# Kernel optimization log

Measured on AMD Instinct MI355X. Metric: run time of the kernel, lower is better.

## Reference

```python
import jax, jax.numpy as jnp
import numpy as np

N, E, D_IN, D_HID, D_OUT = 100000, 1600000, 128, 128, 40

def _sage_pool(x, src, dst, Wp, bp, Ws, Wn, b, n_nodes):
    # DGL SAGEConv 'pool': h_pool = relu(fc_pool(x)); h_neigh = max over in-neighbors;
    # out = fc_self(x) + fc_neigh(h_neigh) + bias
    hp = jax.nn.relu(x @ Wp + bp)                       # [N, d]
    msg = hp[src]                                        # [E, d] gather
    agg = jax.ops.segment_max(msg, dst, num_segments=n_nodes)  # [N, d] scatter-max
    agg = jnp.where(jnp.isfinite(agg), agg, 0.0)         # zero-in-degree nodes -> 0
    return x @ Ws + agg @ Wn + b

def setup_inputs() -> dict:
    key = jax.random.key(0)
    ks = jax.random.split(key, 14)
    def lin(k, i, o):
        return jax.random.normal(k, (i, o), dtype=jnp.float32) / np.sqrt(i)
    return {
        "in_feat": jax.random.normal(ks[0], (N, D_IN), dtype=jnp.float32),
        "src": jax.random.randint(ks[1], (E,), 0, N),
        "dst": jax.random.randint(ks[2], (E,), 0, N),
        "Wp1": lin(ks[3], D_IN, D_IN), "bp1": jnp.zeros((D_IN,), jnp.float32),
        "Ws1": lin(ks[4], D_IN, D_HID), "Wn1": lin(ks[5], D_IN, D_HID),
        "b1": jnp.zeros((D_HID,), jnp.float32),
        "Wp2": lin(ks[6], D_HID, D_HID), "bp2": jnp.zeros((D_HID,), jnp.float32),
        "Ws2": lin(ks[7], D_HID, D_OUT), "Wn2": lin(ks[8], D_HID, D_OUT),
        "b2": jnp.zeros((D_OUT,), jnp.float32),
    }

def reference(in_feat, src, dst, Wp1, bp1, Ws1, Wn1, b1, Wp2, bp2, Ws2, Wn2, b2):
    h = _sage_pool(in_feat, src, dst, Wp1, bp1, Ws1, Wn1, b1, N)
    h = jax.nn.relu(h)
    # dropout is identity at inference (eval mode)
    return _sage_pool(h, src, dst, Wp2, bp2, Ws2, Wn2, b2, N)
```

## Files before the change

kernel.cpp:

```cpp
#include <hip/hip_runtime.h>
#include <stdint.h>

#define NN 100000
#define NE 1600000
#define NB 391

using u16 = unsigned short;
using u32 = unsigned int;

typedef __attribute__((ext_vector_type(8))) short bf16x8;
typedef __attribute__((ext_vector_type(4))) float f32x4;

__device__ inline u16 f2b(float f){
  u32 u = __float_as_uint(f);
  u32 r = (u + 0x7fffu + ((u >> 16) & 1u)) >> 16;
  return (u16)r;
}

__global__ void k_prep(const float* __restrict__ Wp1, const float* __restrict__ Ws1,
                       const float* __restrict__ Wn1, const float* __restrict__ Wp2,
                       const float* __restrict__ Ws2, const float* __restrict__ Wn2,
                       u16* __restrict__ wpT1, u16* __restrict__ wc1T,
                       u16* __restrict__ wpT2, u16* __restrict__ wc2T){
  int i = blockIdx.x * 256 + threadIdx.x;
  if (i < 16384){ int n = i >> 7, k = i & 127;
    wpT1[n*128 + k] = f2b(Wp1[k*128 + n]);
    wpT2[n*128 + k] = f2b(Wp2[k*128 + n]);
  }
  if (i < 32768){ int n = i >> 8, k = i & 255;
    float v = (k < 128) ? Ws1[k*128 + n] : Wn1[(k-128)*128 + n];
    wc1T[n*256 + k] = f2b(v);
  }
  if (i < 12288){ int n = i >> 8, k = i & 255;
    float v = 0.f;
    if (n < 40) v = (k < 128) ? Ws2[k*40 + n] : Wn2[(k-128)*40 + n];
    wc2T[n*256 + k] = f2b(v);
  }
}

__global__ __launch_bounds__(256) void k_cb_hist(const int* __restrict__ dst,
                                                 int* __restrict__ cb){
  __shared__ int h[NB];
  for (int i = threadIdx.x; i < NB; i += 256) h[i] = 0;
  __syncthreads();
  int e0 = blockIdx.x * 8192;
  #pragma unroll 4
  for (int j = 0; j < 32; j++){
    int e = e0 + j * 256 + threadIdx.x;
    if (e < NE) atomicAdd(&h[dst[e] >> 8], 1);
  }
  __syncthreads();
  for (int i = threadIdx.x; i < NB; i += 256)
    if (h[i]) atomicAdd(&cb[i], h[i]);
}

__global__ void k_cb_scan(const int* __restrict__ cb, int* __restrict__ cbo,
                          int* __restrict__ curB){
  if (threadIdx.x == 0 && blockIdx.x == 0){
    int a = 0;
    for (int i = 0; i < NB; i++){ cbo[i] = a; curB[i] = a; a += cb[i]; }
    cbo[NB] = a;
  }
}

__global__ __launch_bounds__(256) void k_part(const int* __restrict__ src,
                                              const int* __restrict__ dst,
                                              int* __restrict__ curB,
                                              int2* __restrict__ part){
  __shared__ int hist[NB], scn[NB], cur[NB], base[NB];
  __shared__ int2 stage[4096];
  const int tid = threadIdx.x;
  const int e0 = blockIdx.x * 4096;
  const int cnt = min(4096, NE - e0);
  for (int i = tid; i < NB; i += 256) hist[i] = 0;
  __syncthreads();
  int2 ed[16];
  #pragma unroll
  for (int j = 0; j < 16; j++){
    int e = e0 + j * 256 + tid;
    if (e < NE){
      ed[j].x = src[e]; ed[j].y = dst[e];
      atomicAdd(&hist[ed[j].y >> 8], 1);
    }
  }
  __syncthreads();
  for (int i = tid; i < NB; i += 256)
    base[i] = hist[i] ? atomicAdd(&curB[i], hist[i]) : 0;
  if (tid == 0){
    int a = 0;
    for (int i = 0; i < NB; i++){ scn[i] = a; cur[i] = a; a += hist[i]; }
  }
  __syncthreads();
  #pragma unroll
  for (int j = 0; j < 16; j++){
    int e = e0 + j * 256 + tid;
    if (e < NE){
      int slot = atomicAdd(&cur[ed[j].y >> 8], 1);
      stage[slot] = ed[j];
    }
  }
  __syncthreads();
  for (int i = tid; i < cnt; i += 256){
    int2 p = stage[i];
    int b = p.y >> 8;
    part[base[b] + (i - scn[b])] = p;
  }
}

__global__ __launch_bounds__(256) void k_bsort(const int2* __restrict__ part,
                                               const int* __restrict__ cbo,
                                               int* __restrict__ rp,
                                               int* __restrict__ esrc){
  __shared__ int cnt[256], sc[256], cur[256];
  const int tid = threadIdx.x;
  const int b = blockIdx.x;
  const int lo = cbo[b], hi = cbo[b + 1];
  cnt[tid] = 0;
  __syncthreads();
  for (int i = lo + tid; i < hi; i += 256)
    atomicAdd(&cnt[part[i].y & 255], 1);
  __syncthreads();
  sc[tid] = cnt[tid];
  __syncthreads();
  #pragma unroll
  for (int off = 1; off < 256; off <<= 1){
    int t = (tid >= off) ? sc[tid - off] : 0;
    __syncthreads();
    sc[tid] += t;
    __syncthreads();
  }
  int ex = sc[tid] - cnt[tid];
  int n = (b << 8) + tid;
  if (n < NN) rp[n] = lo + ex;
  if (b == NB - 1 && tid == 0) rp[NN] = hi;
  cur[tid] = lo + ex;
  __syncthreads();
  for (int i = lo + tid; i < hi; i += 256){
    int2 p = part[i];
    int pos = atomicAdd(&cur[p.y & 255], 1);
    esrc[pos] = p.x;
  }
}

__global__ void k_agg(const u16* __restrict__ hp, const int* __restrict__ rp,
                      const int* __restrict__ esrc, u16* __restrict__ agg){
  int node = blockIdx.x * 4 + (threadIdx.x >> 6);
  if (node >= NN) return;
  const int lane = threadIdx.x & 63;
  const int half = lane >> 5;
  const int l32  = lane & 31;
  const int lo = rp[node], hi = rp[node + 1];
  u32 m0 = 0, m1 = 0;
  for (int i = lo; i < hi; i += 16){
    int s[8];
    #pragma unroll
    for (int j = 0; j < 8; j++){
      int ii = i + 2 * j + half; if (ii >= hi) ii = hi - 1;
      s[j] = esrc[ii];
    }
    uint2 v[8];
    #pragma unroll
    for (int j = 0; j < 8; j++)
      v[j] = *(const uint2*)&hp[(size_t)s[j] * 128 + l32 * 4];
    #pragma unroll
    for (int j = 0; j < 8; j++){
      asm("v_pk_max_u16 %0, %0, %1" : "+v"(m0) : "v"(v[j].x));
      asm("v_pk_max_u16 %0, %0, %1" : "+v"(m1) : "v"(v[j].y));
    }
  }
  u32 t0 = (u32)__shfl_xor((int)m0, 32);
  u32 t1 = (u32)__shfl_xor((int)m1, 32);
  asm("v_pk_max_u16 %0, %0, %1" : "+v"(m0) : "v"(t0));
  asm("v_pk_max_u16 %0, %0, %1" : "+v"(m1) : "v"(t1));
  if (half == 0)
    *(uint2*)&agg[(size_t)node * 128 + l32 * 4] = make_uint2(m0, m1);
}

template<int K, int NOUT, int NOUTR, int BM, int NT,
         bool A1F32, bool HASA2, bool RELU, bool OUTF32>
__global__ __launch_bounds__(NT)
void k_gemm(const void* __restrict__ A1p, const u16* __restrict__ A2,
            const u16* __restrict__ Wt, const float* __restrict__ bias,
            void* __restrict__ outp)
{
  constexpr int KSTEP = 64;
  constexpr int KP = KSTEP + 8;
  constexpr int NTI = NOUT / 16;
  __shared__ u16 A_lds[BM * KP];
  __shared__ u16 W_lds[NOUT * KP];
  const int tid  = threadIdx.x;
  const int row0 = blockIdx.x * BM;
  const int wave = tid >> 6, lane = tid & 63;
  const int koff = (lane >> 4) * 8;
  const u16* Ar = &A_lds[(wave * 16 + (lane & 15)) * KP];

  f32x4 acc[NTI] = {};

  #pragma unroll
  for (int k0 = 0; k0 < K; k0 += KSTEP){
    if (k0) __syncthreads();
    for (int c = tid; c < NOUT * 8; c += NT){
      int n = c >> 3, kc = c & 7;
      *(uint4*)&W_lds[n * KP + kc * 8] = *(const uint4*)&Wt[n * K + k0 + kc * 8];
    }
    if (A1F32 && k0 < 128){
      const float* A = (const float*)A1p;
      for (int c = tid; c < BM * 16; c += NT){
        int rl = c >> 4, kc = c & 15;
        int gr = row0 + rl;
        float4 v = make_float4(0.f, 0.f, 0.f, 0.f);
        if (gr < NN) v = *(const float4*)&A[(size_t)gr * 128 + k0 + kc * 4];
        ushort4 o; o.x = f2b(v.x); o.y = f2b(v.y); o.z = f2b(v.z); o.w = f2b(v.w);
        *(ushort4*)&A_lds[rl * KP + kc * 4] = o;
      }
    } else {
      const u16* A = (HASA2 && k0 >= 128) ? A2 : (const u16*)A1p;
      int cb = (HASA2 && k0 >= 128) ? (k0 - 128) : k0;
      for (int c = tid; c < BM * 8; c += NT){
        int rl = c >> 3, kc = c & 7;
        int gr = row0 + rl;
        uint4 v = make_uint4(0, 0, 0, 0);
        if (gr < NN) v = *(const uint4*)&A[(size_t)gr * 128 + cb + kc * 8];
        *(uint4*)&A_lds[rl * KP + kc * 8] = v;
      }
    }
    __syncthreads();

    bf16x8 af0 = *(const bf16x8*)&Ar[koff];
    bf16x8 af1 = *(const bf16x8*)&Ar[32 + koff];
    #pragma unroll
    for (int nt = 0; nt < NTI; nt++){
      const u16* Wr = &W_lds[(nt * 16 + (lane & 15)) * KP];
      bf16x8 b0 = *(const bf16x8*)&Wr[koff];
      bf16x8 b1 = *(const bf16x8*)&Wr[32 + koff];
      acc[nt] = __builtin_amdgcn_mfma_f32_16x16x32_bf16(af0, b0, acc[nt], 0, 0, 0);
      acc[nt] = __builtin_amdgcn_mfma_f32_16x16x32_bf16(af1, b1, acc[nt], 0, 0, 0);
    }
  }

  const int colb = lane & 15;
  const int rowl = wave * 16 + ((lane >> 4) << 2);
  #pragma unroll
  for (int nt = 0; nt < NTI; nt++){
    int col = nt * 16 + colb;
    if (col >= NOUTR) continue;
    float bv = bias[col];
    #pragma unroll
    for (int r = 0; r < 4; r++){
      int gr = row0 + rowl + r;
      if (gr >= NN) continue;
      float v = acc[nt][r] + bv;
      if (RELU) v = fmaxf(v, 0.f);
      if (OUTF32) ((float*)outp)[(size_t)gr * NOUTR + col] = v;
      else        ((u16*)outp)[(size_t)gr * NOUTR + col] = f2b(v);
    }
  }
}

extern "C" void kernel_launch(void* const* d_in, const int* in_sizes, int n_in,
                              void* d_out, int out_size, void* d_ws, size_t ws_size,
                              hipStream_t stream){
  const float* x   = (const float*)d_in[0];
  const int*   src = (const int*)d_in[1];
  const int*   dst = (const int*)d_in[2];
  const float* Wp1 = (const float*)d_in[3];
  const float* bp1 = (const float*)d_in[4];
  const float* Ws1 = (const float*)d_in[5];
  const float* Wn1 = (const float*)d_in[6];
  const float* b1  = (const float*)d_in[7];
  const float* Wp2 = (const float*)d_in[8];
  const float* bp2 = (const float*)d_in[9];
  const float* Ws2 = (const float*)d_in[10];
  const float* Wn2 = (const float*)d_in[11];
  const float* b2  = (const float*)d_in[12];

  char* ws = (char*)d_ws;
  u16* wpT1 = (u16*)(ws + 0);
  u16* wc1T = (u16*)(ws + 32768);
  u16* wpT2 = (u16*)(ws + 98304);
  u16* wc2T = (u16*)(ws + 131072);
  int* cb   = (int*)(ws + 155648);
  int* cbo  = (int*)(ws + 157696);
  int* curB = (int*)(ws + 159744);
  int* rp   = (int*)(ws + 161792);
  int2* part= (int2*)(ws + 561920);
  u16* h    = (u16*)(ws + 561920);
  int* esrc = (int*)(ws + 26161920);
  u16* hp   = (u16*)(ws + 32561920);
  u16* agg  = (u16*)(ws + 58161920);

  hipMemsetAsync(cb, 0, NB * sizeof(int), stream);
  k_prep<<<128, 256, 0, stream>>>(Wp1, Ws1, Wn1, Wp2, Ws2, Wn2, wpT1, wc1T, wpT2, wc2T);
  k_cb_hist<<<(NE + 8191) / 8192, 256, 0, stream>>>(dst, cb);
  k_cb_scan<<<1, 64, 0, stream>>>(cb, cbo, curB);
  k_part<<<(NE + 4095) / 4096, 256, 0, stream>>>(src, dst, curB, part);
  k_bsort<<<NB, 256, 0, stream>>>(part, cbo, rp, esrc);

  k_gemm<128,128,128, 64,256, true ,false,true ,false>
      <<<(NN + 63) / 64, 256, 0, stream>>>(x, nullptr, wpT1, bp1, hp);
  k_agg<<<(NN + 3) / 4, 256, 0, stream>>>(hp, rp, esrc, agg);
  k_gemm<256,128,128,128,512, true ,true ,true ,false>
      <<<(NN + 127) / 128, 512, 0, stream>>>(x, agg, wc1T, b1, h);
  k_gemm<128,128,128, 64,256, false,false,true ,false>
      <<<(NN + 63) / 64, 256, 0, stream>>>(h, nullptr, wpT2, bp2, hp);
  k_agg<<<(NN + 3) / 4, 256, 0, stream>>>(hp, rp, esrc, agg);
  k_gemm<256, 48, 40,128,512, false,true ,false,true >
      <<<(NN + 127) / 128, 512, 0, stream>>>(h, agg, wc2T, b2, d_out);
}
```

Baseline: 284.1 us.

## Fuse neighbor max-aggregation into the combine GEMM through LDS

The separate gather/segment-max kernel is removed. Each combine-GEMM block now computes the max-aggregated neighbor features for its 128 rows straight into shared memory, then consumes them as the second half of K. This removes the agg buffer's global write and re-read and one launch per layer. In exchange the block carries more LDS (an extra 128x136 tile), and the irregular gather latency now runs inside the GEMM block, with each wave looping serially over its 16 nodes, which may lower occupancy and latency hiding.

```diff
diff --git a/kernel.cpp b/kernel.cpp
--- a/kernel.cpp
+++ b/kernel.cpp
@@ -142,46 +142,11 @@
   }
 }
 
-__global__ void k_agg(const u16* __restrict__ hp, const int* __restrict__ rp,
-                      const int* __restrict__ esrc, u16* __restrict__ agg){
-  int node = blockIdx.x * 4 + (threadIdx.x >> 6);
-  if (node >= NN) return;
-  const int lane = threadIdx.x & 63;
-  const int half = lane >> 5;
-  const int l32  = lane & 31;
-  const int lo = rp[node], hi = rp[node + 1];
-  u32 m0 = 0, m1 = 0;
-  for (int i = lo; i < hi; i += 16){
-    int s[8];
-    #pragma unroll
-    for (int j = 0; j < 8; j++){
-      int ii = i + 2 * j + half; if (ii >= hi) ii = hi - 1;
-      s[j] = esrc[ii];
-    }
-    uint2 v[8];
-    #pragma unroll
-    for (int j = 0; j < 8; j++)
-      v[j] = *(const uint2*)&hp[(size_t)s[j] * 128 + l32 * 4];
-    #pragma unroll
-    for (int j = 0; j < 8; j++){
-      asm("v_pk_max_u16 %0, %0, %1" : "+v"(m0) : "v"(v[j].x));
-      asm("v_pk_max_u16 %0, %0, %1" : "+v"(m1) : "v"(v[j].y));
-    }
-  }
-  u32 t0 = (u32)__shfl_xor((int)m0, 32);
-  u32 t1 = (u32)__shfl_xor((int)m1, 32);
-  asm("v_pk_max_u16 %0, %0, %1" : "+v"(m0) : "v"(t0));
-  asm("v_pk_max_u16 %0, %0, %1" : "+v"(m1) : "v"(t1));
-  if (half == 0)
-    *(uint2*)&agg[(size_t)node * 128 + l32 * 4] = make_uint2(m0, m1);
-}
-
 template<int K, int NOUT, int NOUTR, int BM, int NT,
-         bool A1F32, bool HASA2, bool RELU, bool OUTF32>
+         bool A1F32, bool RELU, bool OUTF32>
 __global__ __launch_bounds__(NT)
-void k_gemm(const void* __restrict__ A1p, const u16* __restrict__ A2,
-            const u16* __restrict__ Wt, const float* __restrict__ bias,
-            void* __restrict__ outp)
+void k_gemm(const void* __restrict__ A1p, const u16* __restrict__ Wt,
+            const float* __restrict__ bias, void* __restrict__ outp)
 {
   constexpr int KSTEP = 64;
   constexpr int KP = KSTEP + 8;
@@ -203,7 +168,7 @@
       int n = c >> 3, kc = c & 7;
       *(uint4*)&W_lds[n * KP + kc * 8] = *(const uint4*)&Wt[n * K + k0 + kc * 8];
     }
-    if (A1F32 && k0 < 128){
+    if (A1F32){
       const float* A = (const float*)A1p;
       for (int c = tid; c < BM * 16; c += NT){
         int rl = c >> 4, kc = c & 15;
@@ -214,13 +179,12 @@
         *(ushort4*)&A_lds[rl * KP + kc * 4] = o;
       }
     } else {
-      const u16* A = (HASA2 && k0 >= 128) ? A2 : (const u16*)A1p;
-      int cb = (HASA2 && k0 >= 128) ? (k0 - 128) : k0;
+      const u16* A = (const u16*)A1p;
       for (int c = tid; c < BM * 8; c += NT){
         int rl = c >> 3, kc = c & 7;
         int gr = row0 + rl;
         uint4 v = make_uint4(0, 0, 0, 0);
-        if (gr < NN) v = *(const uint4*)&A[(size_t)gr * 128 + cb + kc * 8];
+        if (gr < NN) v = *(const uint4*)&A[(size_t)gr * 128 + k0 + kc * 8];
         *(uint4*)&A_lds[rl * KP + kc * 8] = v;
       }
     }
@@ -228,6 +192,130 @@
 
     bf16x8 af0 = *(const bf16x8*)&Ar[koff];
     bf16x8 af1 = *(const bf16x8*)&Ar[32 + koff];
+    #pragma unroll
+    for (int nt = 0; nt < NTI; nt++){
+      const u16* Wr = &W_lds[(nt * 16 + (lane & 15)) * KP];
+      bf16x8 b0 = *(const bf16x8*)&Wr[koff];
+      bf16x8 b1 = *(const bf16x8*)&Wr[32 + koff];
+      acc[nt] = __builtin_amdgcn_mfma_f32_16x16x32_bf16(af0, b0, acc[nt], 0, 0, 0);
+      acc[nt] = __builtin_amdgcn_mfma_f32_16x16x32_bf16(af1, b1, acc[nt], 0, 0, 0);
+    }
+  }
+
+  const int colb = lane & 15;
+  const int rowl = wave * 16 + ((lane >> 4) << 2);
+  #pragma unroll
+  for (int nt = 0; nt < NTI; nt++){
+    int col = nt * 16 + colb;
+    if (col >= NOUTR) continue;
+    float bv = bias[col];
+    #pragma unroll
+    for (int r = 0; r < 4; r++){
+      int gr = row0 + rowl + r;
+      if (gr >= NN) continue;
+      float v = acc[nt][r] + bv;
+      if (RELU) v = fmaxf(v, 0.f);
+      if (OUTF32) ((float*)outp)[(size_t)gr * NOUTR + col] = v;
+      else        ((u16*)outp)[(size_t)gr * NOUTR + col] = f2b(v);
+    }
+  }
+}
+
+template<int NOUT, int NOUTR, bool A1F32, bool RELU, bool OUTF32>
+__global__ __launch_bounds__(512)
+void k_fgemm(const void* __restrict__ A1p, const u16* __restrict__ hp,
+             const int* __restrict__ rp, const int* __restrict__ esrc,
+             const u16* __restrict__ Wt, const float* __restrict__ bias,
+             void* __restrict__ outp)
+{
+  constexpr int BM = 128, NT = 512, KSTEP = 64;
+  constexpr int KP  = KSTEP + 8;
+  constexpr int KP2 = 136;
+  constexpr int NTI = NOUT / 16;
+  __shared__ u16 A_lds[BM * KP];
+  __shared__ u16 W_lds[NOUT * KP];
+  __shared__ u16 G_lds[BM * KP2];
+  const int tid  = threadIdx.x;
+  const int row0 = blockIdx.x * BM;
+  const int wave = tid >> 6, lane = tid & 63;
+  const int half = lane >> 5, l32 = lane & 31;
+  const int koff = (lane >> 4) * 8;
+
+  for (int j = 0; j < 16; j++){
+    int node = row0 + wave * 16 + j;
+    u32 m0 = 0, m1 = 0;
+    if (node < NN){
+      int lo = rp[node], hi = rp[node + 1];
+      for (int i = lo; i < hi; i += 16){
+        int s[8];
+        #pragma unroll
+        for (int t = 0; t < 8; t++){
+          int ii = i + 2 * t + half; if (ii >= hi) ii = hi - 1;
+          s[t] = esrc[ii];
+        }
+        uint2 v[8];
+        #pragma unroll
+        for (int t = 0; t < 8; t++)
+          v[t] = *(const uint2*)&hp[(size_t)s[t] * 128 + l32 * 4];
+        #pragma unroll
+        for (int t = 0; t < 8; t++){
+          asm("v_pk_max_u16 %0, %0, %1" : "+v"(m0) : "v"(v[t].x));
+          asm("v_pk_max_u16 %0, %0, %1" : "+v"(m1) : "v"(v[t].y));
+        }
+      }
+    }
+    u32 t0 = (u32)__shfl_xor((int)m0, 32);
+    u32 t1 = (u32)__shfl_xor((int)m1, 32);
+    asm("v_pk_max_u16 %0, %0, %1" : "+v"(m0) : "v"(t0));
+    asm("v_pk_max_u16 %0, %0, %1" : "+v"(m1) : "v"(t1));
+    if (half == 0)
+      *(uint2*)&G_lds[(wave * 16 + j) * KP2 + l32 * 4] = make_uint2(m0, m1);
+  }
+
+  const u16* Ar = &A_lds[(wave * 16 + (lane & 15)) * KP];
+  const u16* Gr = &G_lds[(wave * 16 + (lane & 15)) * KP2];
+
+  f32x4 acc[NTI] = {};
+
+  #pragma unroll
+  for (int k0 = 0; k0 < 256; k0 += KSTEP){
+    if (k0) __syncthreads();
+    for (int c = tid; c < NOUT * 8; c += NT){
+      int n = c >> 3, kc = c & 7;
+      *(uint4*)&W_lds[n * KP + kc * 8] = *(const uint4*)&Wt[n * 256 + k0 + kc * 8];
+    }
+    if (k0 < 128){
+      if (A1F32){
+        const float* A = (const float*)A1p;
+        for (int c = tid; c < BM * 16; c += NT){
+          int rl = c >> 4, kc = c & 15;
+          int gr = row0 + rl;
+          float4 v = make_float4(0.f, 0.f, 0.f, 0.f);
+          if (gr < NN) v = *(const float4*)&A[(size_t)gr * 128 + k0 + kc * 4];
+          ushort4 o; o.x = f2b(v.x); o.y = f2b(v.y); o.z = f2b(v.z); o.w = f2b(v.w);
+          *(ushort4*)&A_lds[rl * KP + kc * 4] = o;
+        }
+      } else {
+        const u16* A = (const u16*)A1p;
+        for (int c = tid; c < BM * 8; c += NT){
+          int rl = c >> 3, kc = c & 7;
+          int gr = row0 + rl;
+          uint4 v = make_uint4(0, 0, 0, 0);
+          if (gr < NN) v = *(const uint4*)&A[(size_t)gr * 128 + k0 + kc * 8];
+          *(uint4*)&A_lds[rl * KP + kc * 8] = v;
+        }
+      }
+    }
+    __syncthreads();
+
+    bf16x8 af0, af1;
+    if (k0 < 128){
+      af0 = *(const bf16x8*)&Ar[koff];
+      af1 = *(const bf16x8*)&Ar[32 + koff];
+    } else {
+      af0 = *(const bf16x8*)&Gr[(k0 - 128) + koff];
+      af1 = *(const bf16x8*)&Gr[(k0 - 128) + 32 + koff];
+    }
     #pragma unroll
     for (int nt = 0; nt < NTI; nt++){
       const u16* Wr = &W_lds[(nt * 16 + (lane & 15)) * KP];
@@ -287,7 +375,6 @@
   u16* h    = (u16*)(ws + 561920);
   int* esrc = (int*)(ws + 26161920);
   u16* hp   = (u16*)(ws + 32561920);
-  u16* agg  = (u16*)(ws + 58161920);
 
   hipMemsetAsync(cb, 0, NB * sizeof(int), stream);
   k_prep<<<128, 256, 0, stream>>>(Wp1, Ws1, Wn1, Wp2, Ws2, Wn2, wpT1, wc1T, wpT2, wc2T);
@@ -296,14 +383,12 @@
   k_part<<<(NE + 4095) / 4096, 256, 0, stream>>>(src, dst, curB, part);
   k_bsort<<<NB, 256, 0, stream>>>(part, cbo, rp, esrc);
 
-  k_gemm<128,128,128, 64,256, true ,false,true ,false>
-      <<<(NN + 63) / 64, 256, 0, stream>>>(x, nullptr, wpT1, bp1, hp);
-  k_agg<<<(NN + 3) / 4, 256, 0, stream>>>(hp, rp, esrc, agg);
-  k_gemm<256,128,128,128,512, true ,true ,true ,false>
-      <<<(NN + 127) / 128, 512, 0, stream>>>(x, agg, wc1T, b1, h);
-  k_gemm<128,128,128, 64,256, false,false,true ,false>
-      <<<(NN + 63) / 64, 256, 0, stream>>>(h, nullptr, wpT2, bp2, hp);
-  k_agg<<<(NN + 3) / 4, 256, 0, stream>>>(hp, rp, esrc, agg);
-  k_gemm<256, 48, 40,128,512, false,true ,false,true >
-      <<<(NN + 127) / 128, 512, 0, stream>>>(h, agg, wc2T, b2, d_out);
-}
+  k_gemm<128,128,128, 64,256, true ,true ,false>
+      <<<(NN + 63) / 64, 256, 0, stream>>>(x, wpT1, bp1, hp);
+  k_fgemm<128,128, true ,true ,false>
+      <<<(NN + 127) / 128, 512, 0, stream>>>(x, hp, rp, esrc, wc1T, b1, h);
+  k_gemm<128,128,128, 64,256, false,true ,false>
+      <<<(NN + 63) / 64, 256, 0, stream>>>(h, wpT2, bp2, hp);
+  k_fgemm< 48, 40, false,false,true >
+      <<<(NN + 127) / 128, 512, 0, stream>>>(h, hp, rp, esrc, wc2T, b2, d_out);
+}
```

Result: slower. 302.8 us (+6.6%).

## Fuse layer-1 combine GEMM with layer-2 pool GEMM and coarsen CSR buckets

Applied to the files above, without the earlier changes.

Adds a fused kernel that computes h = relu(x@Ws1 + agg@Wn1 + b1), keeps the tile in LDS, and immediately applies the layer-2 pool projection to write hp. This removes one GEMM launch and the re-read of h from global memory. The CSR build also moves to 512-node buckets with parallel LDS scans in place of serial single-thread scans, and the memset is folded into the prep kernel. The first pool GEMM now uses 128-row tiles. The risk is higher register pressure in the fused kernel, and its second-GEMM weight fragments are read directly from global memory.

```diff
diff --git a/kernel.cpp b/kernel.cpp
--- a/kernel.cpp
+++ b/kernel.cpp
@@ -3,7 +3,7 @@
 
 #define NN 100000
 #define NE 1600000
-#define NB 391
+#define NB 196
 
 using u16 = unsigned short;
 using u32 = unsigned int;
@@ -21,8 +21,10 @@
                        const float* __restrict__ Wn1, const float* __restrict__ Wp2,
                        const float* __restrict__ Ws2, const float* __restrict__ Wn2,
                        u16* __restrict__ wpT1, u16* __restrict__ wc1T,
-                       u16* __restrict__ wpT2, u16* __restrict__ wc2T){
+                       u16* __restrict__ wpT2, u16* __restrict__ wc2T,
+                       int* __restrict__ cb){
   int i = blockIdx.x * 256 + threadIdx.x;
+  if (i < NB) cb[i] = 0;
   if (i < 16384){ int n = i >> 7, k = i & 127;
     wpT1[n*128 + k] = f2b(Wp1[k*128 + n]);
     wpT2[n*128 + k] = f2b(Wp2[k*128 + n]);
@@ -47,32 +49,43 @@
   #pragma unroll 4
   for (int j = 0; j < 32; j++){
     int e = e0 + j * 256 + threadIdx.x;
-    if (e < NE) atomicAdd(&h[dst[e] >> 8], 1);
+    if (e < NE) atomicAdd(&h[dst[e] >> 9], 1);
   }
   __syncthreads();
   for (int i = threadIdx.x; i < NB; i += 256)
     if (h[i]) atomicAdd(&cb[i], h[i]);
 }
 
-__global__ void k_cb_scan(const int* __restrict__ cb, int* __restrict__ cbo,
-                          int* __restrict__ curB){
-  if (threadIdx.x == 0 && blockIdx.x == 0){
-    int a = 0;
-    for (int i = 0; i < NB; i++){ cbo[i] = a; curB[i] = a; a += cb[i]; }
-    cbo[NB] = a;
-  }
+__global__ __launch_bounds__(256) void k_cb_scan(const int* __restrict__ cb,
+                                                 int* __restrict__ cbo,
+                                                 int* __restrict__ curB){
+  __shared__ int s[256];
+  int tid = threadIdx.x;
+  int v = (tid < NB) ? cb[tid] : 0;
+  s[tid] = v;
+  __syncthreads();
+  #pragma unroll
+  for (int off = 1; off < 256; off <<= 1){
+    int t = (tid >= off) ? s[tid - off] : 0;
+    __syncthreads();
+    s[tid] += t;
+    __syncthreads();
+  }
+  int ex = s[tid] - v;
+  if (tid < NB){ cbo[tid] = ex; curB[tid] = ex; }
+  if (tid == 255) cbo[NB] = s[255];
 }
 
 __global__ __launch_bounds__(256) void k_part(const int* __restrict__ src,
                                               const int* __restrict__ dst,
                                               int* __restrict__ curB,
                                               int2* __restrict__ part){
-  __shared__ int hist[NB], scn[NB], cur[NB], base[NB];
+  __shared__ int hist[256], scn[256], cur[256], base[256];
   __shared__ int2 stage[4096];
   const int tid = threadIdx.x;
   const int e0 = blockIdx.x * 4096;
   const int cnt = min(4096, NE - e0);
-  for (int i = tid; i < NB; i += 256) hist[i] = 0;
+  hist[tid] = 0;
   __syncthreads();
   int2 ed[16];
   #pragma unroll
@@ -80,64 +93,72 @@
     int e = e0 + j * 256 + tid;
     if (e < NE){
       ed[j].x = src[e]; ed[j].y = dst[e];
-      atomicAdd(&hist[ed[j].y >> 8], 1);
-    }
-  }
-  __syncthreads();
-  for (int i = tid; i < NB; i += 256)
-    base[i] = hist[i] ? atomicAdd(&curB[i], hist[i]) : 0;
-  if (tid == 0){
-    int a = 0;
-    for (int i = 0; i < NB; i++){ scn[i] = a; cur[i] = a; a += hist[i]; }
-  }
+      atomicAdd(&hist[ed[j].y >> 9], 1);
+    }
+  }
+  __syncthreads();
+  int hv = hist[tid];
+  base[tid] = (tid < NB && hv) ? atomicAdd(&curB[tid], hv) : 0;
+  scn[tid] = hv;
+  __syncthreads();
+  #pragma unroll
+  for (int off = 1; off < 256; off <<= 1){
+    int t = (tid >= off) ? scn[tid - off] : 0;
+    __syncthreads();
+    scn[tid] += t;
+    __syncthreads();
+  }
+  int ex = scn[tid] - hv;
+  scn[tid] = ex;
+  cur[tid] = ex;
   __syncthreads();
   #pragma unroll
   for (int j = 0; j < 16; j++){
     int e = e0 + j * 256 + tid;
     if (e < NE){
-      int slot = atomicAdd(&cur[ed[j].y >> 8], 1);
+      int slot = atomicAdd(&cur[ed[j].y >> 9], 1);
       stage[slot] = ed[j];
     }
   }
   __syncthreads();
   for (int i = tid; i < cnt; i += 256){
     int2 p = stage[i];
-    int b = p.y >> 8;
+    int b = p.y >> 9;
     part[base[b] + (i - scn[b])] = p;
   }
 }
 
-__global__ __launch_bounds__(256) void k_bsort(const int2* __restrict__ part,
+__global__ __launch_bounds__(512) void k_bsort(const int2* __restrict__ part,
                                                const int* __restrict__ cbo,
                                                int* __restrict__ rp,
                                                int* __restrict__ esrc){
-  __shared__ int cnt[256], sc[256], cur[256];
+  __shared__ int cnt[512], sc[512], cur[512];
   const int tid = threadIdx.x;
   const int b = blockIdx.x;
   const int lo = cbo[b], hi = cbo[b + 1];
   cnt[tid] = 0;
   __syncthreads();
-  for (int i = lo + tid; i < hi; i += 256)
-    atomicAdd(&cnt[part[i].y & 255], 1);
+  for (int i = lo + tid; i < hi; i += 512)
+    atomicAdd(&cnt[part[i].y & 511], 1);
   __syncthreads();
   sc[tid] = cnt[tid];
   __syncthreads();
   #pragma unroll
-  for (int off = 1; off < 256; off <<= 1){
+  for (int off = 1; off < 512; off <<= 1){
     int t = (tid >= off) ? sc[tid - off] : 0;
     __syncthreads();
     sc[tid] += t;
     __syncthreads();
   }
   int ex = sc[tid] - cnt[tid];
-  int n = (b << 8) + tid;
+  int n = (b << 9) + tid;
   if (n < NN) rp[n] = lo + ex;
   if (b == NB - 1 && tid == 0) rp[NN] = hi;
   cur[tid] = lo + ex;
   __syncthreads();
-  for (int i = lo + tid; i < hi; i += 256){
+  for (int i = lo + tid; i < hi; i += 512){
     int2 p = part[i];
-    int pos = atomicAdd(&cur[p.y & 255], 1);
+    int pos = atomicAdd(&cur[p.y & 511], 1);
     esrc[pos] = p.x;
   }
 }
@@ -215,12 +236,12 @@
       }
     } else {
       const u16* A = (HASA2 && k0 >= 128) ? A2 : (const u16*)A1p;
-      int cb = (HASA2 && k0 >= 128) ? (k0 - 128) : k0;
+      int cb2 = (HASA2 && k0 >= 128) ? (k0 - 128) : k0;
       for (int c = tid; c < BM * 8; c += NT){
         int rl = c >> 3, kc = c & 7;
         int gr = row0 + rl;
         uint4 v = make_uint4(0, 0, 0, 0);
-        if (gr < NN) v = *(const uint4*)&A[(size_t)gr * 128 + cb + kc * 8];
+        if (gr < NN) v = *(const uint4*)&A[(size_t)gr * 128 + cb2 + kc * 8];
         *(uint4*)&A_lds[rl * KP + kc * 8] = v;
       }
     }
@@ -253,6 +274,109 @@
       if (RELU) v = fmaxf(v, 0.f);
       if (OUTF32) ((float*)outp)[(size_t)gr * NOUTR + col] = v;
       else        ((u16*)outp)[(size_t)gr * NOUTR + col] = f2b(v);
+    }
+  }
+}
+
+__global__ __launch_bounds__(512)
+void k_cgemm(const float* __restrict__ x, const u16* __restrict__ agg,
+             const u16* __restrict__ Wc, const float* __restrict__ b1,
+             const u16* __restrict__ wp2T, const float* __restrict__ bp2,
+             u16* __restrict__ h, u16* __restrict__ hp)
+{
+  constexpr int BM = 128, NT = 512, KSTEP = 64, KP = 72, KPB = 136;
+  __shared__ u16 S[128 * KP * 2];
+  u16* A_lds = S;
+  u16* W_lds = S + 128 * KP;
+  const int tid  = threadIdx.x;
+  const int row0 = blockIdx.x * BM;
+  const int wave = tid >> 6, lane = tid & 63;
+  const int koff = (lane >> 4) * 8;
+  const u16* Ar = &A_lds[(wave * 16 + (lane & 15)) * KP];
+
+  f32x4 acc[8] = {};
+
+  #pragma unroll
+  for (int k0 = 0; k0 < 256; k0 += KSTEP){
+    if (k0) __syncthreads();
+    for (int c = tid; c < 128 * 8; c += NT){
+      int n = c >> 3, kc = c & 7;
+      *(uint4*)&W_lds[n * KP + kc * 8] = *(const uint4*)&Wc[n * 256 + k0 + kc * 8];
+    }
+    if (k0 < 128){
+      for (int c = tid; c < BM * 16; c += NT){
+        int rl = c >> 4, kc = c & 15;
+        int gr = row0 + rl;
+        float4 v = make_float4(0.f, 0.f, 0.f, 0.f);
+        if (gr < NN) v = *(const float4*)&x[(size_t)gr * 128 + k0 + kc * 4];
+        ushort4 o; o.x = f2b(v.x); o.y = f2b(v.y); o.z = f2b(v.z); o.w = f2b(v.w);
+        *(ushort4*)&A_lds[rl * KP + kc * 4] = o;
+      }
+    } else {
+      for (int c = tid; c < BM * 8; c += NT){
+        int rl = c >> 3, kc = c & 7;
+        int gr = row0 + rl;
+        uint4 v = make_uint4(0, 0, 0, 0);
+        if (gr < NN) v = *(const uint4*)&agg[(size_t)gr * 128 + (k0 - 128) + kc * 8];
+        *(uint4*)&A_lds[rl * KP + kc * 8] = v;
+      }
+    }
+    __syncthreads();
+
+    bf16x8 af0 = *(const bf16x8*)&Ar[koff];
+    bf16x8 af1 = *(const bf16x8*)&Ar[32 + koff];
+    #pragma unroll
+    for (int nt = 0; nt < 8; nt++){
+      const u16* Wr = &W_lds[(nt * 16 + (lane & 15)) * KP];
+      bf16x8 b0 = *(const bf16x8*)&Wr[koff];
+      bf16x8 b1 = *(const bf16x8*)&Wr[32 + koff];
+      acc[nt] = __builtin_amdgcn_mfma_f32_16x16x32_bf16(af0, b0, acc[nt], 0, 0, 0);
+      acc[nt] = __builtin_amdgcn_mfma_f32_16x16x32_bf16(af1, b1, acc[nt], 0, 0, 0);
+    }
+  }
+
+  __syncthreads();
+
+  const int colb = lane & 15;
+  const int q4   = (lane >> 4) << 2;
+  const int rowl = wave * 16 + q4;
+  #pragma unroll
+  for (int nt = 0; nt < 8; nt++){
+    int col = nt * 16 + colb;
+    float bv = b1[col];
+    #pragma unroll
+    for (int r = 0; r < 4; r++){
+      float v = fmaxf(acc[nt][r] + bv, 0.f);
+      u16 hb = f2b(v);
+      S[(rowl + r) * KPB + col] = hb;
+      int gr = row0 + rowl + r;
+      if (gr < NN) h[(size_t)gr * 128 + col] = hb;
+    }
+  }
+  const int bandrow = (wave * 16 + (lane & 15)) * KPB;
+  bf16x8 af[4];
+  #pragma unroll
+  for (int kf = 0; kf < 4; kf++)
+    af[kf] = *(const bf16x8*)&S[bandrow + kf * 32 + koff];
+
+  f32x4 acc2[8] = {};
+  #pragma unroll
+  for (int nt = 0; nt < 8; nt++){
+    #pragma unroll
+    for (int kf = 0; kf < 4; kf++){
+      bf16x8 bf = *(const bf16x8*)&wp2T[(nt * 16 + colb) * 128 + kf * 32 + koff];
+      acc2[nt] = __builtin_amdgcn_mfma_f32_16x16x32_bf16(af[kf], bf, acc2[nt], 0, 0, 0);
+    }
+  }
+  #pragma unroll
+  for (int nt = 0; nt < 8; nt++){
+    int col = nt * 16 + colb;
+    float bv = bp2[col];
+    #pragma unroll
+    for (int r = 0; r < 4; r++){
+      int gr = row0 + rowl + r;
+      if (gr < NN)
+        hp[(size_t)gr * 128 + col] = f2b(fmaxf(acc2[nt][r] + bv, 0.f));
     }
   }
 }
@@ -289,20 +413,17 @@
   u16* hp   = (u16*)(ws + 32561920);
   u16* agg  = (u16*)(ws + 58161920);
 
-  hipMemsetAsync(cb, 0, NB * sizeof(int), stream);
-  k_prep<<<128, 256, 0, stream>>>(Wp1, Ws1, Wn1, Wp2, Ws2, Wn2, wpT1, wc1T, wpT2, wc2T);
+  k_prep<<<128, 256, 0, stream>>>(Wp1, Ws1, Wn1, Wp2, Ws2, Wn2,
+                                  wpT1, wc1T, wpT2, wc2T, cb);
   k_cb_hist<<<(NE + 8191) / 8192, 256, 0, stream>>>(dst, cb);
-  k_cb_scan<<<1, 64, 0, stream>>>(cb, cbo, curB);
+  k_cb_scan<<<1, 256, 0, stream>>>(cb, cbo, curB);
   k_part<<<(NE + 4095) / 4096, 256, 0, stream>>>(src, dst, curB, part);
-  k_bsort<<<NB, 256, 0, stream>>>(part, cbo, rp, esrc);
-
-  k_gemm<128,128,128, 64,256, true ,false,true ,false>
-      <<<(NN + 63) / 64, 256, 0, stream>>>(x, nullptr, wpT1, bp1, hp);
+  k_bsort<<<NB, 512, 0, stream>>>(part, cbo, rp, esrc);
+
+  k_gemm<128,128,128,128,512, true ,false,true ,false>
+      <<<(NN + 127) / 128, 512, 0, stream>>>(x, nullptr, wpT1, bp1, hp);
   k_agg<<<(NN + 3) / 4, 256, 0, stream>>>(hp, rp, esrc, agg);
-  k_gemm<256,128,128,128,512, true ,true ,true ,false>
-      <<<(NN + 127) / 128, 512, 0, stream>>>(x, agg, wc1T, b1, h);
-  k_gemm<128,128,128, 64,256, false,false,true ,false>
-      <<<(NN + 63) / 64, 256, 0, stream>>>(h, nullptr, wpT2, bp2, hp);
+  k_cgemm<<<(NN + 127) / 128, 512, 0, stream>>>(x, agg, wc1T, b1, wpT2, bp2, h, hp);
   k_agg<<<(NN + 3) / 4, 256, 0, stream>>>(hp, rp, esrc, agg);
   k_gemm<256, 48, 40,128,512, false,true ,false,true >
       <<<(NN + 127) / 128, 512, 0, stream>>>(h, agg, wc2T, b2, d_out);
```

New measurement: 268.6 us. -5.5%, faster.
